# Kernel optimization log

Measured on AMD Instinct MI355X. Metric: run time of the kernel, lower is better.

The kernel has to match this reference:

```python
import jax, jax.numpy as jnp
import numpy as np

B, S, D = 4, 2048, 1024

def setup_inputs() -> dict:
    key = jax.random.key(0)
    ks = jax.random.split(key, 10)
    sc = 1.0 / np.sqrt(D)
    return {
        "x": jax.random.normal(ks[0], (B, S, D), dtype=jnp.float32),
        "y": jax.random.normal(ks[1], (B, S, D), dtype=jnp.float32),
        "Wq": jax.random.normal(ks[2], (D, D), dtype=jnp.float32) * sc,
        "bq": jnp.zeros((D,), dtype=jnp.float32),
        "Wk": jax.random.normal(ks[3], (D, D), dtype=jnp.float32) * sc,
        "bk": jnp.zeros((D,), dtype=jnp.float32),
        "Wv": jax.random.normal(ks[4], (D, D), dtype=jnp.float32) * sc,
        "bv": jnp.zeros((D,), dtype=jnp.float32),
        "Wr": jax.random.normal(ks[5], (D, D), dtype=jnp.float32) * sc,
        "br": jnp.zeros((D,), dtype=jnp.float32),
    }

def reference(x, y, Wq, bq, Wk, bk, Wv, bv, Wr, br):
    # Dense projections
    Q = jnp.einsum('bsd,de->bse', x, Wq) + bq
    K = jnp.einsum('bsd,de->bse', y, Wk) + bk
    V = jnp.einsum('bsd,de->bse', y, Wv) + bv
    # learned cosine feature map on keys
    K_hat = jnp.cos(jnp.einsum('bsd,dr->bsr', K, Wr) + br)
    # full softmax attention with feature-mapped keys
    scores = jnp.einsum('bqr,bkr->bqk', Q, K_hat)  # [B, S, S]
    probs = jax.nn.softmax(scores, axis=-1)
    return jnp.einsum('bqk,bkd->bqd', probs, V)
```

## Files before the change

### kernel.cpp

```cpp
#include <hip/hip_runtime.h>
#include <hip/hip_bf16.h>
#include <math.h>

#define B_ 4
#define S_ 2048
#define D_ 1024
#define M_ (B_*S_)
#define MBYTE (1024ull*1024ull)

typedef __attribute__((ext_vector_type(8))) _Float16 f16x8;
typedef __attribute__((ext_vector_type(4))) float f32x4;
typedef __attribute__((ext_vector_type(8))) unsigned short us8;
typedef unsigned short us;

__device__ inline us f2h(float f) {
    union { _Float16 h; us u; } x;
    x.h = (_Float16)f;
    return x.u;
}
__device__ inline float h2f(us u) {
    union { us u; _Float16 h; } x; x.u = u;
    return (float)x.h;
}

__device__ inline void gload16(const us* g, us* l) {
    __builtin_amdgcn_global_load_lds(
        (const __attribute__((address_space(1))) unsigned int*)g,
        (__attribute__((address_space(3))) unsigned int*)l, 16, 0, 0);
}

template<int DO_LO>
__global__ __launch_bounds__(256)
void cast2_k(const float* __restrict__ in, us* __restrict__ hi, us* __restrict__ lo) {
    const size_t i = ((size_t)blockIdx.x * 256 + threadIdx.x) * 4;
    const float4 v = *(const float4*)&in[i];
    ushort4 h;
    h.x = f2h(v.x); h.y = f2h(v.y); h.z = f2h(v.z); h.w = f2h(v.w);
    *(ushort4*)&hi[i] = h;
    if (DO_LO) {
        ushort4 l;
        l.x = f2h(v.x - h2f(h.x)); l.y = f2h(v.y - h2f(h.y));
        l.z = f2h(v.z - h2f(h.z)); l.w = f2h(v.w - h2f(h.w));
        *(ushort4*)&lo[i] = l;
    }
}

template<int DO_LO>
__global__ __launch_bounds__(256)
void wsplit_k(const float* __restrict__ W, us* __restrict__ Wt1, us* __restrict__ Wt2) {
    __shared__ float t[64][65];
    const int tid = threadIdx.x;
    const int k0 = blockIdx.x*64, n0 = blockIdx.y*64;
    #pragma unroll
    for (int i = 0; i < 4; ++i) {
        const int c = i*256 + tid;
        const int row = c >> 4, col = (c & 15) * 4;
        const float4 v = *(const float4*)&W[(size_t)(k0+row)*D_ + n0+col];
        t[row][col]=v.x; t[row][col+1]=v.y; t[row][col+2]=v.z; t[row][col+3]=v.w;
    }
    __syncthreads();
    #pragma unroll
    for (int i = 0; i < 4; ++i) {
        const int c = i*256 + tid;
        const int n = c >> 4, k = (c & 15) * 4;
        float f[4] = { t[k][n], t[k+1][n], t[k+2][n], t[k+3][n] };
        ushort4 h;
        h.x=f2h(f[0]); h.y=f2h(f[1]); h.z=f2h(f[2]); h.w=f2h(f[3]);
        *(ushort4*)&Wt1[(size_t)(n0+n)*D_ + k0+k] = h;
        if (DO_LO) {
            ushort4 l;
            l.x=f2h(f[0]-h2f(h.x)); l.y=f2h(f[1]-h2f(h.y));
            l.z=f2h(f[2]-h2f(h.z)); l.w=f2h(f[3]-h2f(h.w));
            *(ushort4*)&Wt2[(size_t)(n0+n)*D_ + k0+k] = l;
        }
    }
}

__global__ __launch_bounds__(256)
void wreduce_k(const float* __restrict__ Wp, us* __restrict__ W1, us* __restrict__ W2) {
    const size_t i = ((size_t)blockIdx.x * 256 + threadIdx.x) * 4;
    float4 s = *(const float4*)&Wp[i];
    #pragma unroll
    for (int z = 1; z < 8; ++z) {
        const float4 v = *(const float4*)&Wp[(size_t)z*D_*D_ + i];
        s.x += v.x; s.y += v.y; s.z += v.z; s.w += v.w;
    }
    ushort4 h, l;
    h.x=f2h(s.x); h.y=f2h(s.y); h.z=f2h(s.z); h.w=f2h(s.w);
    l.x=f2h(s.x-h2f(h.x)); l.y=f2h(s.y-h2f(h.y));
    l.z=f2h(s.z-h2f(h.z)); l.w=f2h(s.w-h2f(h.w));
    *(ushort4*)&W1[i] = h;
    *(ushort4*)&W2[i] = l;
}

__global__ __launch_bounds__(256)
void bpinit_k(const float* __restrict__ br, float* __restrict__ bp) {
    const int r = blockIdx.x * 256 + threadIdx.x;
    bp[r] = br[r];
}
__global__ __launch_bounds__(256)
void bprime_k(const float* __restrict__ bk, const float* __restrict__ Wr,
              float* __restrict__ bp) {
    const int r = blockIdx.x * 256 + threadIdx.x;
    const int e0 = blockIdx.y * 64;
    float a0 = 0.f, a1 = 0.f, a2 = 0.f, a3 = 0.f;
    for (int e = e0; e < e0 + 64; e += 4) {
        a0 += bk[e+0] * Wr[(size_t)(e+0)*D_ + r];
        a1 += bk[e+1] * Wr[(size_t)(e+1)*D_ + r];
        a2 += bk[e+2] * Wr[(size_t)(e+2)*D_ + r];
        a3 += bk[e+3] * Wr[(size_t)(e+3)*D_ + r];
    }
    atomicAdd(&bp[r], (a0 + a1) + (a2 + a3));
}

template<int Nv, int Kv, int SPLIT, int EPI, int KS>
__global__ __launch_bounds__(256)
void gemm_bt_k(const us* __restrict__ A1, const us* __restrict__ A2,
               const us* __restrict__ B1, const us* __restrict__ B2,
               const float* __restrict__ bias, void* __restrict__ Cv,
               long sA, long sB, long sC) {
    __shared__ us smem[4*128*64];
    const int tid = threadIdx.x;
    const us* A1b = A1 + (size_t)blockIdx.z * sA;
    const us* A2b = SPLIT ? A2 + (size_t)blockIdx.z * sA : nullptr;
    const us* B1b = B1 + (size_t)blockIdx.z * sB;
    const us* B2b = SPLIT ? B2 + (size_t)blockIdx.z * sB : nullptr;
    const int m0 = blockIdx.x * 128, n0 = blockIdx.y * 128;
    const int lane = tid & 63, w = tid >> 6;
    const int mw = (w >> 1) * 64, nw = (w & 1) * 64;
    const int lr = lane & 15, lq = lane >> 4;

    const int crow = tid >> 3;
    const int ccol = (tid & 7) * 8;

    f32x4 acc[4][4];
    #pragma unroll
    for (int i = 0; i < 4; ++i)
        #pragma unroll
        for (int j = 0; j < 4; ++j)
            acc[i][j] = (f32x4){0.f, 0.f, 0.f, 0.f};

    int kc0 = 0, kc1 = Kv;
    if (KS > 1) {
        const int kchunk = Kv / KS;
        kc0 = blockIdx.z * kchunk;
        kc1 = kc0 + kchunk;
    }

    if constexpr (SPLIT) {
        us* As  = smem;
        us* As2 = smem + 128*64;
        us* Bs  = smem + 2*128*64;
        us* Bs2 = smem + 3*128*64;
        for (int kc = kc0; kc < kc1; kc += 64) {
            #pragma unroll
            for (int i = 0; i < 4; ++i) {
                const int r = crow + i * 32;
                const size_t off = (size_t)(i*256 + tid) * 8;
                gload16(&A1b[(size_t)(m0 + r) * Kv + kc + ccol], &As[off]);
                gload16(&B1b[(size_t)(n0 + r) * Kv + kc + ccol], &Bs[off]);
                gload16(&A2b[(size_t)(m0 + r) * Kv + kc + ccol], &As2[off]);
                gload16(&B2b[(size_t)(n0 + r) * Kv + kc + ccol], &Bs2[off]);
            }
            __syncthreads();
            #pragma unroll
            for (int kk = 0; kk < 64; kk += 32) {
                f16x8 a1[4], b1[4], a2[4], b2[4];
                #pragma unroll
                for (int i = 0; i < 4; ++i) {
                    a1[i] = *(const f16x8*)&As [(mw + i*16 + lr) * 64 + kk + lq*8];
                    a2[i] = *(const f16x8*)&As2[(mw + i*16 + lr) * 64 + kk + lq*8];
                }
                #pragma unroll
                for (int j = 0; j < 4; ++j) {
                    b1[j] = *(const f16x8*)&Bs [(nw + j*16 + lr) * 64 + kk + lq*8];
                    b2[j] = *(const f16x8*)&Bs2[(nw + j*16 + lr) * 64 + kk + lq*8];
                }
                #pragma unroll
                for (int i = 0; i < 4; ++i)
                    #pragma unroll
                    for (int j = 0; j < 4; ++j) {
                        acc[i][j] = __builtin_amdgcn_mfma_f32_16x16x32_f16(a2[i], b1[j], acc[i][j], 0, 0, 0);
                        acc[i][j] = __builtin_amdgcn_mfma_f32_16x16x32_f16(a1[i], b2[j], acc[i][j], 0, 0, 0);
                        acc[i][j] = __builtin_amdgcn_mfma_f32_16x16x32_f16(a1[i], b1[j], acc[i][j], 0, 0, 0);
                    }
            }
            __syncthreads();
        }
    } else {
        constexpr int BUFE = 2*128*64;
        auto STAGE = [&](int b, int kc) {
            us* dst = smem + b * BUFE;
            #pragma unroll
            for (int i = 0; i < 4; ++i) {
                const int r = crow + i * 32;
                const size_t off = (size_t)(i*256 + tid) * 8;
                gload16(&A1b[(size_t)(m0 + r) * Kv + kc + ccol], &dst[off]);
                gload16(&B1b[(size_t)(n0 + r) * Kv + kc + ccol], &dst[128*64 + off]);
            }
        };
        STAGE(0, kc0);
        int cur = 0;
        for (int kc = kc0; kc < kc1; kc += 64) {
            const bool pf = (kc + 64 < kc1);
            if (pf) {
                STAGE(cur ^ 1, kc + 64);
                asm volatile("s_waitcnt vmcnt(8)" ::: "memory");
            } else {
                asm volatile("s_waitcnt vmcnt(0)" ::: "memory");
            }
            __builtin_amdgcn_s_barrier();
            const us* As_ = smem + cur * BUFE;
            const us* Bs_ = As_ + 128*64;
            #pragma unroll
            for (int kk = 0; kk < 64; kk += 32) {
                f16x8 a1[4], b1[4];
                #pragma unroll
                for (int i = 0; i < 4; ++i)
                    a1[i] = *(const f16x8*)&As_[(mw + i*16 + lr) * 64 + kk + lq*8];
                #pragma unroll
                for (int j = 0; j < 4; ++j)
                    b1[j] = *(const f16x8*)&Bs_[(nw + j*16 + lr) * 64 + kk + lq*8];
                #pragma unroll
                for (int i = 0; i < 4; ++i)
                    #pragma unroll
                    for (int j = 0; j < 4; ++j)
                        acc[i][j] = __builtin_amdgcn_mfma_f32_16x16x32_f16(a1[i], b1[j], acc[i][j], 0, 0, 0);
            }
            __builtin_amdgcn_s_barrier();
            cur ^= 1;
        }
    }

    float* slab = (float*)smem + (size_t)w * 2048;
    const int lrow0 = lane >> 3, cb = (lane & 7) * 8;
    #pragma unroll
    for (int p = 0; p < 2; ++p) {
        #pragma unroll
        for (int ii = 0; ii < 2; ++ii) {
            const int i = p*2 + ii;
            #pragma unroll
            for (int j = 0; j < 4; ++j)
                #pragma unroll
                for (int r = 0; r < 4; ++r)
                    slab[(ii*16 + lq*4 + r)*64 + j*16 + lr] = acc[i][j][r];
        }
        __syncthreads();
        #pragma unroll
        for (int t = 0; t < 4; ++t) {
            const int lrow = t*8 + lrow0;
            const int grow = m0 + mw + p*32 + lrow;
            const int gcol = n0 + nw + cb;
            const size_t idx = (size_t)grow * Nv + gcol;
            float v[8];
            #pragma unroll
            for (int u = 0; u < 8; ++u) v[u] = slab[lrow*64 + cb + u];
            if (EPI == 0) {
                float* Cf = (float*)Cv + (size_t)blockIdx.z * sC;
                float4 o0 = {v[0],v[1],v[2],v[3]}, o1 = {v[4],v[5],v[6],v[7]};
                *(float4*)&Cf[idx] = o0;
                *(float4*)&Cf[idx+4] = o1;
            } else if (EPI == 1 || EPI == 2) {
                us* Ch = (us*)Cv + (size_t)blockIdx.z * sC;
                us8 o;
                #pragma unroll
                for (int u = 0; u < 8; ++u) {
                    const float tv = v[u] + (bias ? bias[gcol + u] : 0.f);
                    o[u] = f2h(EPI == 2 ? cosf(tv) : tv);
                }
                *(us8*)&Ch[idx] = o;
            } else {
                us* Ch = (us*)Cv + (size_t)blockIdx.z * sC;
                const float rb = bias ? bias[grow] : 0.f;
                us8 o;
                #pragma unroll
                for (int u = 0; u < 8; ++u) o[u] = f2h(v[u] + rb);
                *(us8*)&Ch[idx] = o;
            }
        }
        __syncthreads();
    }
}

__global__ __launch_bounds__(256)
void softmax_k(const float* __restrict__ S, us* __restrict__ P) {
    __shared__ float red[8];
    const int tid = threadIdx.x;
    const int lane = tid & 63, w = tid >> 6;
    const float* row = S + (size_t)blockIdx.x * S_;

    const float4 v0 = *(const float4*)&row[tid*8];
    const float4 v1 = *(const float4*)&row[tid*8 + 4];
    float e[8] = {v0.x, v0.y, v0.z, v0.w, v1.x, v1.y, v1.z, v1.w};

    float mx = e[0];
    #pragma unroll
    for (int j = 1; j < 8; ++j) mx = fmaxf(mx, e[j]);
    #pragma unroll
    for (int off = 1; off < 64; off <<= 1) mx = fmaxf(mx, __shfl_xor(mx, off));
    if (lane == 0) red[w] = mx;
    __syncthreads();
    mx = fmaxf(fmaxf(red[0], red[1]), fmaxf(red[2], red[3]));

    float sum = 0.f;
    #pragma unroll
    for (int j = 0; j < 8; ++j) { e[j] = __expf(e[j] - mx); sum += e[j]; }
    #pragma unroll
    for (int off = 1; off < 64; off <<= 1) sum += __shfl_xor(sum, off);
    if (lane == 0) red[4 + w] = sum;
    __syncthreads();
    const float inv = 1.0f / (red[4] + red[5] + red[6] + red[7]);

    us8 o;
    #pragma unroll
    for (int j = 0; j < 8; ++j) o[j] = f2h(e[j] * inv);
    *(us8*)&P[(size_t)blockIdx.x * S_ + tid*8] = o;
}

extern "C" void kernel_launch(void* const* d_in, const int* in_sizes, int n_in,
                              void* d_out, int out_size, void* d_ws, size_t ws_size,
                              hipStream_t stream) {
    const float* x  = (const float*)d_in[0];
    const float* y  = (const float*)d_in[1];
    const float* Wq = (const float*)d_in[2];
    const float* bq = (const float*)d_in[3];
    const float* Wk = (const float*)d_in[4];
    const float* bk = (const float*)d_in[5];
    const float* Wv = (const float*)d_in[6];
    const float* bv = (const float*)d_in[7];
    const float* Wr = (const float*)d_in[8];
    const float* br = (const float*)d_in[9];
    float* out = (float*)d_out;

    char* wsb = (char*)d_ws;
    us*    y1   = (us*)(wsb +  0*MBYTE);
    us*    y2   = (us*)(wsb + 16*MBYTE);
    us*    xh   = (us*)(wsb + 16*MBYTE);
    us*    Pb   = (us*)(wsb + 16*MBYTE);
    float* Wp   = (float*)(wsb + 32*MBYTE);
    us*    Qb   = (us*)(wsb + 32*MBYTE);
    us*    P23  = (us*)(wsb + 32*MBYTE);
    us*    Kh   = (us*)(wsb + 48*MBYTE);
    us*    Wkf1 = (us*)(wsb + 64*MBYTE);
    us*    Wkf2 = (us*)(wsb + 66*MBYTE);
    us*    Wr1  = (us*)(wsb + 68*MBYTE);
    us*    Wr2  = (us*)(wsb + 70*MBYTE);
    us*    WT1  = (us*)(wsb + 72*MBYTE);
    us*    WT2  = (us*)(wsb + 74*MBYTE);
    float* bp   = (float*)(wsb + 76*MBYTE);
    us*    Wq1  = (us*)(wsb + 64*MBYTE);
    float* S2   = (float*)(wsb + 64*MBYTE);
    us*    Vt   = (us*)(wsb + 64*MBYTE);
    us*    Wv1  = (us*)(wsb + 80*MBYTE);

    const dim3 bb(256);
    const dim3 gcast(M_*D_/1024), gcastW(D_*D_/1024), gw(16,16);
    const dim3 gproj(M_/128, D_/128);

    cast2_k<1><<<gcast, bb, 0, stream>>>(y, y1, y2);
    cast2_k<1><<<gcastW, bb, 0, stream>>>(Wk, Wkf1, Wkf2);
    wsplit_k<1><<<gw, bb, 0, stream>>>(Wr, Wr1, Wr2);
    bpinit_k<<<dim3(D_/256), bb, 0, stream>>>(br, bp);
    bprime_k<<<dim3(D_/256, 16), bb, 0, stream>>>(bk, Wr, bp);
    gemm_bt_k<D_, D_, 1, 0, 8><<<dim3(D_/128, D_/128, 8), bb, 0, stream>>>(
        Wr1, Wr2, Wkf1, Wkf2, nullptr, (void*)Wp, 0, 0, (long)D_*D_);
    wreduce_k<<<dim3(D_*D_/1024), bb, 0, stream>>>(Wp, WT1, WT2);

    gemm_bt_k<D_, D_, 1, 2, 1><<<gproj, bb, 0, stream>>>(
        y1, y2, WT1, WT2, bp, (void*)Kh, 0, 0, 0);

    cast2_k<0><<<gcast, bb, 0, stream>>>(x, xh, nullptr);
    wsplit_k<0><<<gw, bb, 0, stream>>>(Wq, Wq1, nullptr);
    gemm_bt_k<D_, D_, 0, 1, 1><<<gproj, bb, 0, stream>>>(
        xh, nullptr, Wq1, nullptr, bq, (void*)Qb, 0, 0, 0);

    gemm_bt_k<S_, D_, 0, 0, 1><<<dim3(S_/128, S_/128, 2), bb, 0, stream>>>(
        Qb, nullptr, Kh, nullptr, nullptr,
        (void*)S2, (long)S_*D_, (long)S_*D_, (long)S_*S_);
    softmax_k<<<dim3(2*S_), bb, 0, stream>>>(S2, Pb);
    gemm_bt_k<S_, D_, 0, 0, 1><<<dim3(S_/128, S_/128, 2), bb, 0, stream>>>(
        Qb + 2*(size_t)S_*D_, nullptr, Kh + 2*(size_t)S_*D_, nullptr, nullptr,
        (void*)S2, (long)S_*D_, (long)S_*D_, (long)S_*S_);
    softmax_k<<<dim3(2*S_), bb, 0, stream>>>(S2, P23);

    wsplit_k<0><<<gw, bb, 0, stream>>>(Wv, Wv1, nullptr);
    gemm_bt_k<S_, D_, 0, 4, 1><<<dim3(D_/128, S_/128, B_), bb, 0, stream>>>(
        Wv1, nullptr, y1, nullptr, bv, (void*)Vt,
        0, (long)S_*D_, (long)D_*S_);

    gemm_bt_k<D_, S_, 0, 0, 1><<<dim3(S_/128, D_/128, B_), bb, 0, stream>>>(
        Pb, nullptr, Vt, nullptr, nullptr, (void*)out,
        (long)S_*S_, (long)D_*S_, (long)S_*D_);
}
```

Baseline: 471.9 us.

## Double-buffer split-precision GEMM path with BK=32 prefetch stages

```diff
diff --git a/kernel.cpp b/kernel.cpp
--- a/kernel.cpp
+++ b/kernel.cpp
@@ -148,44 +148,58 @@
     }
 
     if constexpr (SPLIT) {
-        us* As  = smem;
-        us* As2 = smem + 128*64;
-        us* Bs  = smem + 2*128*64;
-        us* Bs2 = smem + 3*128*64;
-        for (int kc = kc0; kc < kc1; kc += 64) {
+        constexpr int BKS  = 32;
+        constexpr int MATE = 128 * BKS;
+        constexpr int BUFE = 4 * MATE;
+        const int r0 = tid >> 2;
+        const int c0 = (tid & 3) * 8;
+        auto STAGE = [&](int b, int kc) {
+            us* dst = smem + b * BUFE;
+            #pragma unroll
+            for (int i = 0; i < 2; ++i) {
+                const int r = r0 + i * 64;
+                const size_t off = (size_t)(i*256 + tid) * 8;
+                gload16(&A1b[(size_t)(m0 + r) * Kv + kc + c0], &dst[off]);
+                gload16(&B1b[(size_t)(n0 + r) * Kv + kc + c0], &dst[MATE + off]);
+                gload16(&A2b[(size_t)(m0 + r) * Kv + kc + c0], &dst[2*MATE + off]);
+                gload16(&B2b[(size_t)(n0 + r) * Kv + kc + c0], &dst[3*MATE + off]);
+            }
+        };
+        STAGE(0, kc0);
+        int cur = 0;
+        for (int kc = kc0; kc < kc1; kc += BKS) {
+            if (kc + BKS < kc1) {
+                STAGE(cur ^ 1, kc + BKS);
+                asm volatile("s_waitcnt vmcnt(8)" ::: "memory");
+            } else {
+                asm volatile("s_waitcnt vmcnt(0)" ::: "memory");
+            }
+            __builtin_amdgcn_s_barrier();
+            const us* As_  = smem + cur * BUFE;
+            const us* Bs_  = As_ + MATE;
+            const us* As2_ = As_ + 2*MATE;
+            const us* Bs2_ = As_ + 3*MATE;
+            f16x8 a1[4], b1[4], a2[4], b2[4];
             #pragma unroll
             for (int i = 0; i < 4; ++i) {
-                const int r = crow + i * 32;
-                const size_t off = (size_t)(i*256 + tid) * 8;
-                gload16(&A1b[(size_t)(m0 + r) * Kv + kc + ccol], &As[off]);
-                gload16(&B1b[(size_t)(n0 + r) * Kv + kc + ccol], &Bs[off]);
-                gload16(&A2b[(size_t)(m0 + r) * Kv + kc + ccol], &As2[off]);
-                gload16(&B2b[(size_t)(n0 + r) * Kv + kc + ccol], &Bs2[off]);
-            }
-            __syncthreads();
-            #pragma unroll
-            for (int kk = 0; kk < 64; kk += 32) {
-                f16x8 a1[4], b1[4], a2[4], b2[4];
-                #pragma unroll
-                for (int i = 0; i < 4; ++i) {
-                    a1[i] = *(const f16x8*)&As [(mw + i*16 + lr) * 64 + kk + lq*8];
-                    a2[i] = *(const f16x8*)&As2[(mw + i*16 + lr) * 64 + kk + lq*8];
+                a1[i] = *(const f16x8*)&As_ [(mw + i*16 + lr) * BKS + lq*8];
+                a2[i] = *(const f16x8*)&As2_[(mw + i*16 + lr) * BKS + lq*8];
+            }
+            #pragma unroll
+            for (int j = 0; j < 4; ++j) {
+                b1[j] = *(const f16x8*)&Bs_ [(nw + j*16 + lr) * BKS + lq*8];
+                b2[j] = *(const f16x8*)&Bs2_[(nw + j*16 + lr) * BKS + lq*8];
+            }
+            #pragma unroll
+            for (int i = 0; i < 4; ++i)
+                #pragma unroll
+                for (int j = 0; j < 4; ++j) {
+                    acc[i][j] = __builtin_amdgcn_mfma_f32_16x16x32_f16(a2[i], b1[j], acc[i][j], 0, 0, 0);
+                    acc[i][j] = __builtin_amdgcn_mfma_f32_16x16x32_f16(a1[i], b2[j], acc[i][j], 0, 0, 0);
+                    acc[i][j] = __builtin_amdgcn_mfma_f32_16x16x32_f16(a1[i], b1[j], acc[i][j], 0, 0, 0);
                 }
-                #pragma unroll
-                for (int j = 0; j < 4; ++j) {
-                    b1[j] = *(const f16x8*)&Bs [(nw + j*16 + lr) * 64 + kk + lq*8];
-                    b2[j] = *(const f16x8*)&Bs2[(nw + j*16 + lr) * 64 + kk + lq*8];
-                }
-                #pragma unroll
-                for (int i = 0; i < 4; ++i)
-                    #pragma unroll
-                    for (int j = 0; j < 4; ++j) {
-                        acc[i][j] = __builtin_amdgcn_mfma_f32_16x16x32_f16(a2[i], b1[j], acc[i][j], 0, 0, 0);
-                        acc[i][j] = __builtin_amdgcn_mfma_f32_16x16x32_f16(a1[i], b2[j], acc[i][j], 0, 0, 0);
-                        acc[i][j] = __builtin_amdgcn_mfma_f32_16x16x32_f16(a1[i], b1[j], acc[i][j], 0, 0, 0);
-                    }
-            }
-            __syncthreads();
+            __builtin_amdgcn_s_barrier();
+            cur ^= 1;
         }
     } else {
         constexpr int BUFE = 2*128*64;
```

Measured after the change: 425.2 us. -9.9%, faster.
